# Optimization experiments

Measured on AMD Instinct MI355X. Metric: run time of the kernel, lower is better.

## Reference

```python
import jax, jax.numpy as jnp
import numpy as np

N_NODES = 100000
N_EDGES = 400000
DIMS = 384
LEAKY_SLOPE = 0.01  # torch LeakyReLU default


def _gcn_conv(x, src, dst, W, b, n_nodes):
    """PyG GCNConv: add self-loops, symmetric deg^{-1/2} normalization,
    linear transform, scatter-add aggregation to target nodes, bias."""
    loop = jnp.arange(n_nodes, dtype=src.dtype)
    src_a = jnp.concatenate([src, loop])
    dst_a = jnp.concatenate([dst, loop])
    deg = jax.ops.segment_sum(jnp.ones_like(dst_a, dtype=x.dtype), dst_a,
                              num_segments=n_nodes)
    dinv = jnp.where(deg > 0, jax.lax.rsqrt(deg), 0.0)
    norm = dinv[src_a] * dinv[dst_a]  # [E+N]
    h = x @ W  # [N, out]
    msg = norm[:, None] * h[src_a]  # gather + scale, [E+N, out]
    out = jax.ops.segment_sum(msg, dst_a, num_segments=n_nodes)  # scatter-add
    return out + b


def _leaky_relu(x):
    return jnp.where(x >= 0, x, LEAKY_SLOPE * x)


def setup_inputs() -> dict:
    key = jax.random.key(0)
    ks = jax.random.split(key, 8)
    d = DIMS
    x = jax.random.normal(ks[0], (N_NODES, d), dtype=jnp.float32)
    edge_index = jax.random.randint(ks[1], (2, N_EDGES), 0, N_NODES, dtype=jnp.int32)
    s1 = 1.0 / np.sqrt(d)
    s2 = 1.0 / np.sqrt(2 * d)
    W1 = jax.random.uniform(ks[2], (d, d), jnp.float32, -s1, s1)
    b1 = jnp.zeros((d,), jnp.float32)
    W2 = jax.random.uniform(ks[3], (2 * d, d), jnp.float32, -s2, s2)
    b2 = jnp.zeros((d,), jnp.float32)
    Wp = jax.random.uniform(ks[4], (d, 1), jnp.float32, -s1, s1)
    bp = jax.random.uniform(ks[5], (1,), jnp.float32, -s1, s1)
    return {"x": x, "edge_index": edge_index, "W1": W1, "b1": b1,
            "W2": W2, "b2": b2, "Wp": Wp, "bp": bp}


def reference(x, edge_index, W1, b1, W2, b2, Wp, bp):
    src, dst = edge_index[0], edge_index[1]
    n = x.shape[0]
    y = _gcn_conv(x, src, dst, W1, b1, n)            # [N, d]
    y = _leaky_relu(jnp.concatenate([x, y], axis=-1))  # [N, 2d]
    z = _leaky_relu(_gcn_conv(y, src, dst, W2, b2, n))  # [N, d]
    a = z @ Wp + bp                                   # [N, 1] pooler
    return (z, a)
```

## Files before the change

kernel.cpp:

```cpp
#include <hip/hip_runtime.h>

#define DIMS 384
#define SLOPE 0.01f

typedef __attribute__((ext_vector_type(8))) short s16x8;
typedef __attribute__((ext_vector_type(8))) unsigned short u16x8;
typedef __attribute__((ext_vector_type(4))) float f32x4;

typedef __attribute__((address_space(1))) const void gld_src_t;
typedef __attribute__((address_space(3))) void lds_dst_t;
#define GLL16(g, l) __builtin_amdgcn_global_load_lds((gld_src_t*)(g), (lds_dst_t*)(l), 16, 0, 0)

__device__ __forceinline__ unsigned short f2bf(float f) {
  unsigned u = __float_as_uint(f);
  unsigned r = (u + 0x7FFFu + ((u >> 16) & 1u)) >> 16;
  return (unsigned short)r;
}

__device__ __forceinline__ float bf2f(unsigned short u) {
  return __uint_as_float((unsigned)u << 16);
}

__device__ __forceinline__ float leaky(float f) { return f >= 0.f ? f : SLOPE * f; }


__global__ void count_kernel(const int* __restrict__ dst, int* __restrict__ cnt, int E) {
  int e = blockIdx.x * blockDim.x + threadIdx.x;
  if (e < E) atomicAdd(&cnt[dst[e]], 1);
}

__global__ void dinv_kernel(const int* __restrict__ cnt, float* __restrict__ dinv, int n) {
  int i = blockIdx.x * blockDim.x + threadIdx.x;
  if (i < n) dinv[i] = 1.0f / sqrtf((float)(cnt[i] + 1));
}

__global__ void scan1_kernel(const int* __restrict__ cnt, int* __restrict__ off,
                             int* __restrict__ bsum, int n) {
  __shared__ int s[256];
  int tid = threadIdx.x, gid = blockIdx.x * 256 + tid;
  int v = gid < n ? cnt[gid] : 0;
  s[tid] = v;
  __syncthreads();
  for (int o = 1; o < 256; o <<= 1) {
    int t = tid >= o ? s[tid - o] : 0;
    __syncthreads();
    s[tid] += t;
    __syncthreads();
  }
  if (gid < n) off[gid] = s[tid] - v;
  if (tid == 255) bsum[blockIdx.x] = s[255];
}

__global__ void scan2_kernel(const int* __restrict__ bsum, int* __restrict__ boff, int nb) {
  __shared__ int s[512];
  int tid = threadIdx.x;
  int v = tid < nb ? bsum[tid] : 0;
  s[tid] = v;
  __syncthreads();
  for (int o = 1; o < 512; o <<= 1) {
    int t = tid >= o ? s[tid - o] : 0;
    __syncthreads();
    s[tid] += t;
    __syncthreads();
  }
  if (tid < nb) boff[tid] = s[tid] - v;
}

__global__ void scan3_kernel(int* __restrict__ off, const int* __restrict__ boff,
                             int* __restrict__ cursor, int n, int E) {
  int gid = blockIdx.x * 256 + threadIdx.x;
  if (gid < n) {
    int v = off[gid] + boff[gid >> 8];
    off[gid] = v;
    cursor[gid] = v;
  }
  if (gid == 0) off[n] = E;
}

__global__ void fill_kernel(const int* __restrict__ src, const int* __restrict__ dst,
                            const float* __restrict__ dinv, int* __restrict__ cursor,
                            int* __restrict__ csr_s, float* __restrict__ csr_w, int E) {
  int e = blockIdx.x * blockDim.x + threadIdx.x;
  if (e >= E) return;
  int d = dst[e], s = src[e];
  int p = atomicAdd(&cursor[d], 1);
  csr_s[p] = s;
  csr_w[p] = dinv[s] * dinv[d];
}

__global__ void wt_kernel(const float* __restrict__ W, unsigned short* __restrict__ Wt, int K) {
  int idx = blockIdx.x * blockDim.x + threadIdx.x;
  if (idx >= K * DIMS) return;
  int k = idx / DIMS, nn = idx - k * DIMS;
  Wt[nn * K + k] = f2bf(W[idx]);
}

__global__ void xprep_kernel(const float* __restrict__ X, unsigned short* __restrict__ Xb,
                             unsigned short* __restrict__ XbL, int total8) {
  int i = blockIdx.x * blockDim.x + threadIdx.x;
  if (i >= total8) return;
  const float4* p = (const float4*)(X + (size_t)i * 8);
  float4 a = p[0], b = p[1];
  float f[8] = {a.x, a.y, a.z, a.w, b.x, b.y, b.z, b.w};
  u16x8 r, l;
#pragma unroll
  for (int j = 0; j < 8; j++) {
    r[j] = f2bf(f[j]);
    l[j] = f2bf(leaky(f[j]));
  }
  *(u16x8*)(Xb + (size_t)i * 8) = r;
  *(u16x8*)(XbL + (size_t)i * 8) = l;
}


template <int LAYER>
__launch_bounds__(256, 4)
__global__ void gemm_kernel(const unsigned short* __restrict__ A1,
                            const unsigned short* __restrict__ A2,
                            const unsigned short* __restrict__ Wt,
                            void* __restrict__ Hout, int M, int K) {
  __shared__ unsigned short As[128 * 64];
  __shared__ unsigned short Bs[128 * 64];
  const int tid = threadIdx.x;
  const int lane = tid & 63;
  const int wave = tid >> 6;
  const int wr = (wave >> 1) * 64;
  const int wc = (wave & 1) * 64;
  const int row0 = blockIdx.x * 128;
  const int n0 = blockIdx.y * 128;
  const int fr = lane & 15;
  const int kq = (lane >> 4) * 8;

  f32x4 acc[4][4] = {};

  for (int k0 = 0; k0 < K; k0 += 64) {
    __syncthreads();
    const unsigned short* Asrc;
    int ka;
    if (LAYER == 2 && k0 >= DIMS) {
      Asrc = A2;
      ka = k0 - DIMS;
    } else {
      Asrc = A1;
      ka = k0;
    }
#pragma unroll
    for (int i = 0; i < 4; i++) {
      const int g = i * 256 + tid;
      const int r = g >> 3;
      const int c = (g & 7) * 8;
      GLL16(Asrc + (size_t)(row0 + r) * DIMS + ka + c, &As[g * 8]);
    }
#pragma unroll
    for (int i = 0; i < 4; i++) {
      const int g = i * 256 + tid;
      const int r = g >> 3;
      const int c = (g & 7) * 8;
      GLL16(Wt + (size_t)(n0 + r) * K + k0 + c, &Bs[g * 8]);
    }
    __syncthreads();

#pragma unroll
    for (int h = 0; h < 2; h++) {
      s16x8 av[4], bv[4];
#pragma unroll
      for (int m = 0; m < 4; m++)
        av[m] = *(const s16x8*)&As[(wr + m * 16 + fr) * 64 + h * 32 + kq];
#pragma unroll
      for (int n = 0; n < 4; n++)
        bv[n] = *(const s16x8*)&Bs[(wc + n * 16 + fr) * 64 + h * 32 + kq];
#pragma unroll
      for (int m = 0; m < 4; m++)
#pragma unroll
        for (int n = 0; n < 4; n++)
          acc[m][n] = __builtin_amdgcn_mfma_f32_16x16x32_bf16(av[m], bv[n], acc[m][n], 0, 0, 0);
    }
  }

  const int rq = (lane >> 4) * 4;
#pragma unroll
  for (int m = 0; m < 4; m++) {
#pragma unroll
    for (int n = 0; n < 4; n++) {
      const int col = n0 + wc + n * 16 + fr;
#pragma unroll
      for (int j = 0; j < 4; j++) {
        const int row = row0 + wr + m * 16 + rq + j;
        if (row < M) {
          if (LAYER == 1)
            ((unsigned short*)Hout)[(size_t)row * DIMS + col] = f2bf(acc[m][n][j]);
          else
            ((float*)Hout)[(size_t)row * DIMS + col] = acc[m][n][j];
        }
      }
    }
  }
}


__global__ void agg1_kernel(const unsigned short* __restrict__ H, const float* __restrict__ bias,
                            const float* __restrict__ dinv, const int* __restrict__ off,
                            const int* __restrict__ csr_s, const float* __restrict__ csr_w,
                            unsigned short* __restrict__ Y, int n) {
  const int wid = (blockIdx.x * blockDim.x + threadIdx.x) >> 6;
  const int lane = threadIdx.x & 63;
  if (wid >= n) return;
  const float ds = dinv[wid];
  const float ws = ds * ds;
  const unsigned short* hr = H + (size_t)wid * DIMS;
  float acc[6];
#pragma unroll
  for (int j = 0; j < 3; j++) {
    const int d = 2 * lane + 128 * j;
    unsigned v = *(const unsigned*)(hr + d);
    acc[2 * j] = bias[d] + ws * bf2f((unsigned short)v);
    acc[2 * j + 1] = bias[d + 1] + ws * bf2f((unsigned short)(v >> 16));
  }
  const int e1 = off[wid + 1];
  for (int e = off[wid]; e < e1; e++) {
    const int s = csr_s[e];
    const float w = csr_w[e];
    const unsigned short* hs = H + (size_t)s * DIMS;
#pragma unroll
    for (int j = 0; j < 3; j++) {
      unsigned v = *(const unsigned*)(hs + 2 * lane + 128 * j);
      acc[2 * j] += w * bf2f((unsigned short)v);
      acc[2 * j + 1] += w * bf2f((unsigned short)(v >> 16));
    }
  }
  unsigned short* o = Y + (size_t)wid * DIMS;
#pragma unroll
  for (int j = 0; j < 3; j++) {
    unsigned lo = f2bf(leaky(acc[2 * j]));
    unsigned hi = f2bf(leaky(acc[2 * j + 1]));
    *(unsigned*)(o + 2 * lane + 128 * j) = lo | (hi << 16);
  }
}


__global__ void agg2_kernel(const float* __restrict__ H, const float* __restrict__ bias,
                            const float* __restrict__ dinv, const int* __restrict__ off,
                            const int* __restrict__ csr_s, const float* __restrict__ csr_w,
                            float* __restrict__ Z, const float* __restrict__ Wp,
                            const float* __restrict__ bp, float* __restrict__ A, int n) {
  const int wid = (blockIdx.x * blockDim.x + threadIdx.x) >> 6;
  const int lane = threadIdx.x & 63;
  if (wid >= n) return;
  const float ds = dinv[wid];
  const float ws = ds * ds;
  const float2* hr = (const float2*)(H + (size_t)wid * DIMS);
  float acc[6];
#pragma unroll
  for (int j = 0; j < 3; j++) {
    const int d = 2 * (lane + 64 * j);
    float2 v = hr[lane + 64 * j];
    acc[2 * j] = bias[d] + ws * v.x;
    acc[2 * j + 1] = bias[d + 1] + ws * v.y;
  }
  const int e1 = off[wid + 1];
  for (int e = off[wid]; e < e1; e++) {
    const int s = csr_s[e];
    const float w = csr_w[e];
    const float2* hs = (const float2*)(H + (size_t)s * DIMS);
#pragma unroll
    for (int j = 0; j < 3; j++) {
      float2 v = hs[lane + 64 * j];
      acc[2 * j] += w * v.x;
      acc[2 * j + 1] += w * v.y;
    }
  }
  float2* zr = (float2*)(Z + (size_t)wid * DIMS);
  float dot = 0.f;
#pragma unroll
  for (int j = 0; j < 3; j++) {
    float z0 = leaky(acc[2 * j]);
    float z1 = leaky(acc[2 * j + 1]);
    float2 wp = ((const float2*)Wp)[lane + 64 * j];
    zr[lane + 64 * j] = make_float2(z0, z1);
    dot += z0 * wp.x + z1 * wp.y;
  }
#pragma unroll
  for (int o = 32; o > 0; o >>= 1) dot += __shfl_xor(dot, o);
  if (lane == 0) A[wid] = dot + bp[0];
}


extern "C" void kernel_launch(void* const* d_in, const int* in_sizes, int n_in,
                              void* d_out, int out_size, void* d_ws, size_t ws_size,
                              hipStream_t stream) {
  const float* x = (const float*)d_in[0];
  const int* ei = (const int*)d_in[1];
  const float* W1 = (const float*)d_in[2];
  const float* b1 = (const float*)d_in[3];
  const float* W2 = (const float*)d_in[4];
  const float* b2 = (const float*)d_in[5];
  const float* Wp = (const float*)d_in[6];
  const float* bp = (const float*)d_in[7];
  const int N = in_sizes[0] / DIMS;
  const int E = in_sizes[1] / 2;
  const int* src = ei;
  const int* dst = ei + E;
  const int NP = N + 128;

  char* p = (char*)d_ws;
  auto alloc = [&](size_t bytes) {
    char* r = p;
    p += (bytes + 255) & ~(size_t)255;
    return r;
  };
  char* regionA = alloc(2 * (size_t)NP * DIMS * 2);
  unsigned short* Xb = (unsigned short*)regionA;
  unsigned short* H1 = (unsigned short*)(regionA + (size_t)NP * DIMS * 2);
  float* H2 = (float*)regionA;
  unsigned short* XbL = (unsigned short*)alloc((size_t)NP * DIMS * 2);
  unsigned short* YBL = (unsigned short*)alloc((size_t)NP * DIMS * 2);
  float* dinv = (float*)alloc((size_t)N * 4);
  int* cnt = (int*)alloc((size_t)N * 4);
  int* off = (int*)alloc((size_t)(N + 1) * 4);
  int* cursor = (int*)alloc((size_t)N * 4);
  int* bsum = (int*)alloc(4096);
  int* boff = (int*)alloc(4096);
  int* csr_s = (int*)alloc((size_t)E * 4);
  float* csr_w = (float*)alloc((size_t)E * 4);
  unsigned short* Wt1 = (unsigned short*)alloc((size_t)DIMS * DIMS * 2);
  unsigned short* Wt2 = (unsigned short*)alloc((size_t)DIMS * 2 * DIMS * 2);

  float* z = (float*)d_out;
  float* a = z + (size_t)N * DIMS;

  const int nbN = (N + 255) / 256;
  const int nbE = (E + 255) / 256;

  hipMemsetAsync(cnt, 0, (size_t)N * 4, stream);
  count_kernel<<<nbE, 256, 0, stream>>>(dst, cnt, E);
  dinv_kernel<<<nbN, 256, 0, stream>>>(cnt, dinv, N);
  scan1_kernel<<<nbN, 256, 0, stream>>>(cnt, off, bsum, N);
  scan2_kernel<<<1, 512, 0, stream>>>(bsum, boff, nbN);
  scan3_kernel<<<nbN, 256, 0, stream>>>(off, boff, cursor, N, E);
  fill_kernel<<<nbE, 256, 0, stream>>>(src, dst, dinv, cursor, csr_s, csr_w, E);
  wt_kernel<<<(DIMS * DIMS + 255) / 256, 256, 0, stream>>>(W1, Wt1, DIMS);
  wt_kernel<<<(2 * DIMS * DIMS + 255) / 256, 256, 0, stream>>>(W2, Wt2, 2 * DIMS);
  const int total8 = N * DIMS / 8;
  xprep_kernel<<<(total8 + 255) / 256, 256, 0, stream>>>(x, Xb, XbL, total8);

  dim3 gg((N + 127) / 128, DIMS / 128);
  gemm_kernel<1><<<gg, 256, 0, stream>>>(Xb, nullptr, Wt1, H1, N, DIMS);
  agg1_kernel<<<(N + 3) / 4, 256, 0, stream>>>(H1, b1, dinv, off, csr_s, csr_w, YBL, N);
  gemm_kernel<2><<<gg, 256, 0, stream>>>(XbL, YBL, Wt2, H2, N, 2 * DIMS);
  agg2_kernel<<<(N + 3) / 4, 256, 0, stream>>>(H2, b2, dinv, off, csr_s, csr_w, z, Wp, bp, a, N);
}
```

Baseline: 486.0 us.

## Store layer-2 features in bf16, replace scan with atomic offsets, unroll aggregation

The layer-2 GEMM output is now stored in bf16 instead of fp32, which halves the bytes gathered per edge in the second aggregation. The three-kernel prefix scan is replaced by a single kernel that reserves each node's CSR segment with an atomicAdd on a global counter, so segments are no longer in node order. Both aggregation kernels are merged into one template that processes two edges per iteration for more loads in flight, and the final z output uses nontemporal stores. The costs are lower precision in the layer-2 messages and scattered CSR locality from the atomic ordering.

```diff
diff --git a/kernel.cpp b/kernel.cpp
--- a/kernel.cpp
+++ b/kernel.cpp
@@ -6,6 +6,7 @@
 typedef __attribute__((ext_vector_type(8))) short s16x8;
 typedef __attribute__((ext_vector_type(8))) unsigned short u16x8;
 typedef __attribute__((ext_vector_type(4))) float f32x4;
+typedef __attribute__((ext_vector_type(2))) float f32x2;
 
 typedef __attribute__((address_space(1))) const void gld_src_t;
 typedef __attribute__((address_space(3))) void lds_dst_t;
@@ -29,52 +30,16 @@
   if (e < E) atomicAdd(&cnt[dst[e]], 1);
 }
 
-__global__ void dinv_kernel(const int* __restrict__ cnt, float* __restrict__ dinv, int n) {
+__global__ void node_prep_kernel(const int* __restrict__ cnt, int* __restrict__ tot,
+                                 float* __restrict__ dinv, int* __restrict__ off,
+                                 int* __restrict__ cursor, int n) {
   int i = blockIdx.x * blockDim.x + threadIdx.x;
-  if (i < n) dinv[i] = 1.0f / sqrtf((float)(cnt[i] + 1));
-}
-
-__global__ void scan1_kernel(const int* __restrict__ cnt, int* __restrict__ off,
-                             int* __restrict__ bsum, int n) {
-  __shared__ int s[256];
-  int tid = threadIdx.x, gid = blockIdx.x * 256 + tid;
-  int v = gid < n ? cnt[gid] : 0;
-  s[tid] = v;
-  __syncthreads();
-  for (int o = 1; o < 256; o <<= 1) {
-    int t = tid >= o ? s[tid - o] : 0;
-    __syncthreads();
-    s[tid] += t;
-    __syncthreads();
-  }
-  if (gid < n) off[gid] = s[tid] - v;
-  if (tid == 255) bsum[blockIdx.x] = s[255];
-}
-
-__global__ void scan2_kernel(const int* __restrict__ bsum, int* __restrict__ boff, int nb) {
-  __shared__ int s[512];
-  int tid = threadIdx.x;
-  int v = tid < nb ? bsum[tid] : 0;
-  s[tid] = v;
-  __syncthreads();
-  for (int o = 1; o < 512; o <<= 1) {
-    int t = tid >= o ? s[tid - o] : 0;
-    __syncthreads();
-    s[tid] += t;
-    __syncthreads();
-  }
-  if (tid < nb) boff[tid] = s[tid] - v;
-}
-
-__global__ void scan3_kernel(int* __restrict__ off, const int* __restrict__ boff,
-                             int* __restrict__ cursor, int n, int E) {
-  int gid = blockIdx.x * 256 + threadIdx.x;
-  if (gid < n) {
-    int v = off[gid] + boff[gid >> 8];
-    off[gid] = v;
-    cursor[gid] = v;
-  }
-  if (gid == 0) off[n] = E;
+  if (i >= n) return;
+  int c = cnt[i];
+  dinv[i] = 1.0f / sqrtf((float)(c + 1));
+  int o = atomicAdd(tot, c);
+  off[i] = o;
+  cursor[i] = o;
 }
 
 __global__ void fill_kernel(const int* __restrict__ src, const int* __restrict__ dst,
@@ -118,7 +83,7 @@
 __global__ void gemm_kernel(const unsigned short* __restrict__ A1,
                             const unsigned short* __restrict__ A2,
                             const unsigned short* __restrict__ Wt,
-                            void* __restrict__ Hout, int M, int K) {
+                            unsigned short* __restrict__ Hout, int M, int K) {
   __shared__ unsigned short As[128 * 64];
   __shared__ unsigned short Bs[128 * 64];
   const int tid = threadIdx.x;
@@ -186,22 +151,20 @@
 #pragma unroll
       for (int j = 0; j < 4; j++) {
         const int row = row0 + wr + m * 16 + rq + j;
-        if (row < M) {
-          if (LAYER == 1)
-            ((unsigned short*)Hout)[(size_t)row * DIMS + col] = f2bf(acc[m][n][j]);
-          else
-            ((float*)Hout)[(size_t)row * DIMS + col] = acc[m][n][j];
-        }
+        if (row < M) Hout[(size_t)row * DIMS + col] = f2bf(acc[m][n][j]);
       }
     }
   }
 }
 
 
-__global__ void agg1_kernel(const unsigned short* __restrict__ H, const float* __restrict__ bias,
-                            const float* __restrict__ dinv, const int* __restrict__ off,
-                            const int* __restrict__ csr_s, const float* __restrict__ csr_w,
-                            unsigned short* __restrict__ Y, int n) {
+template <int MODE>
+__global__ void agg_kernel(const unsigned short* __restrict__ H, const float* __restrict__ bias,
+                           const float* __restrict__ dinv, const int* __restrict__ off,
+                           const int* __restrict__ cnt, const int* __restrict__ csr_s,
+                           const float* __restrict__ csr_w, void* __restrict__ outp,
+                           const float* __restrict__ Wp, const float* __restrict__ bp,
+                           float* __restrict__ A, int n) {
   const int wid = (blockIdx.x * blockDim.x + threadIdx.x) >> 6;
   const int lane = threadIdx.x & 63;
   if (wid >= n) return;
@@ -216,8 +179,28 @@
     acc[2 * j] = bias[d] + ws * bf2f((unsigned short)v);
     acc[2 * j + 1] = bias[d + 1] + ws * bf2f((unsigned short)(v >> 16));
   }
-  const int e1 = off[wid + 1];
-  for (int e = off[wid]; e < e1; e++) {
+  const int e0 = off[wid];
+  const int e1 = e0 + cnt[wid];
+  int e = e0;
+  for (; e + 2 <= e1; e += 2) {
+    const int sA = csr_s[e], sB = csr_s[e + 1];
+    const float wA = csr_w[e], wB = csr_w[e + 1];
+    const unsigned short* hA = H + (size_t)sA * DIMS;
+    const unsigned short* hB = H + (size_t)sB * DIMS;
+    unsigned vA[3], vB[3];
+#pragma unroll
+    for (int j = 0; j < 3; j++) vA[j] = *(const unsigned*)(hA + 2 * lane + 128 * j);
+#pragma unroll
+    for (int j = 0; j < 3; j++) vB[j] = *(const unsigned*)(hB + 2 * lane + 128 * j);
+#pragma unroll
+    for (int j = 0; j < 3; j++) {
+      acc[2 * j] += wA * bf2f((unsigned short)vA[j]);
+      acc[2 * j + 1] += wA * bf2f((unsigned short)(vA[j] >> 16));
+      acc[2 * j] += wB * bf2f((unsigned short)vB[j]);
+      acc[2 * j + 1] += wB * bf2f((unsigned short)(vB[j] >> 16));
+    }
+  }
+  if (e < e1) {
     const int s = csr_s[e];
     const float w = csr_w[e];
     const unsigned short* hs = H + (size_t)s * DIMS;
@@ -228,60 +211,30 @@
       acc[2 * j + 1] += w * bf2f((unsigned short)(v >> 16));
     }
   }
-  unsigned short* o = Y + (size_t)wid * DIMS;
-#pragma unroll
-  for (int j = 0; j < 3; j++) {
-    unsigned lo = f2bf(leaky(acc[2 * j]));
-    unsigned hi = f2bf(leaky(acc[2 * j + 1]));
-    *(unsigned*)(o + 2 * lane + 128 * j) = lo | (hi << 16);
-  }
-}
-
-
-__global__ void agg2_kernel(const float* __restrict__ H, const float* __restrict__ bias,
-                            const float* __restrict__ dinv, const int* __restrict__ off,
-                            const int* __restrict__ csr_s, const float* __restrict__ csr_w,
-                            float* __restrict__ Z, const float* __restrict__ Wp,
-                            const float* __restrict__ bp, float* __restrict__ A, int n) {
-  const int wid = (blockIdx.x * blockDim.x + threadIdx.x) >> 6;
-  const int lane = threadIdx.x & 63;
-  if (wid >= n) return;
-  const float ds = dinv[wid];
-  const float ws = ds * ds;
-  const float2* hr = (const float2*)(H + (size_t)wid * DIMS);
-  float acc[6];
-#pragma unroll
-  for (int j = 0; j < 3; j++) {
-    const int d = 2 * (lane + 64 * j);
-    float2 v = hr[lane + 64 * j];
-    acc[2 * j] = bias[d] + ws * v.x;
-    acc[2 * j + 1] = bias[d + 1] + ws * v.y;
-  }
-  const int e1 = off[wid + 1];
-  for (int e = off[wid]; e < e1; e++) {
-    const int s = csr_s[e];
-    const float w = csr_w[e];
-    const float2* hs = (const float2*)(H + (size_t)s * DIMS);
+  if (MODE == 1) {
+    unsigned short* o = (unsigned short*)outp + (size_t)wid * DIMS;
 #pragma unroll
     for (int j = 0; j < 3; j++) {
-      float2 v = hs[lane + 64 * j];
-      acc[2 * j] += w * v.x;
-      acc[2 * j + 1] += w * v.y;
-    }
-  }
-  float2* zr = (float2*)(Z + (size_t)wid * DIMS);
-  float dot = 0.f;
-#pragma unroll
-  for (int j = 0; j < 3; j++) {
-    float z0 = leaky(acc[2 * j]);
-    float z1 = leaky(acc[2 * j + 1]);
-    float2 wp = ((const float2*)Wp)[lane + 64 * j];
-    zr[lane + 64 * j] = make_float2(z0, z1);
-    dot += z0 * wp.x + z1 * wp.y;
-  }
-#pragma unroll
-  for (int o = 32; o > 0; o >>= 1) dot += __shfl_xor(dot, o);
-  if (lane == 0) A[wid] = dot + bp[0];
+      unsigned lo = f2bf(leaky(acc[2 * j]));
+      unsigned hi = f2bf(leaky(acc[2 * j + 1]));
+      *(unsigned*)(o + 2 * lane + 128 * j) = lo | (hi << 16);
+    }
+  } else {
+    float* Z = (float*)outp + (size_t)wid * DIMS;
+    float dot = 0.f;
+#pragma unroll
+    for (int j = 0; j < 3; j++) {
+      float z0 = leaky(acc[2 * j]);
+      float z1 = leaky(acc[2 * j + 1]);
+      f32x2 wp = *(const f32x2*)(Wp + 2 * lane + 128 * j);
+      f32x2 zv = {z0, z1};
+      __builtin_nontemporal_store(zv, (f32x2*)(Z + 2 * lane + 128 * j));
+      dot += z0 * wp.x + z1 * wp.y;
+    }
+#pragma unroll
+    for (int o = 32; o > 0; o >>= 1) dot += __shfl_xor(dot, o);
+    if (lane == 0) A[wid] = dot + bp[0];
+  }
 }
 
 
@@ -311,15 +264,14 @@
   char* regionA = alloc(2 * (size_t)NP * DIMS * 2);
   unsigned short* Xb = (unsigned short*)regionA;
   unsigned short* H1 = (unsigned short*)(regionA + (size_t)NP * DIMS * 2);
-  float* H2 = (float*)regionA;
+  unsigned short* H2 = (unsigned short*)regionA;
   unsigned short* XbL = (unsigned short*)alloc((size_t)NP * DIMS * 2);
   unsigned short* YBL = (unsigned short*)alloc((size_t)NP * DIMS * 2);
   float* dinv = (float*)alloc((size_t)N * 4);
-  int* cnt = (int*)alloc((size_t)N * 4);
-  int* off = (int*)alloc((size_t)(N + 1) * 4);
+  int* cnt = (int*)alloc((size_t)(N + 1) * 4);
+  int* tot = cnt + N;
+  int* off = (int*)alloc((size_t)N * 4);
   int* cursor = (int*)alloc((size_t)N * 4);
-  int* bsum = (int*)alloc(4096);
-  int* boff = (int*)alloc(4096);
   int* csr_s = (int*)alloc((size_t)E * 4);
   float* csr_w = (float*)alloc((size_t)E * 4);
   unsigned short* Wt1 = (unsigned short*)alloc((size_t)DIMS * DIMS * 2);
@@ -331,12 +283,9 @@
   const int nbN = (N + 255) / 256;
   const int nbE = (E + 255) / 256;
 
-  hipMemsetAsync(cnt, 0, (size_t)N * 4, stream);
+  hipMemsetAsync(cnt, 0, (size_t)(N + 1) * 4, stream);
   count_kernel<<<nbE, 256, 0, stream>>>(dst, cnt, E);
-  dinv_kernel<<<nbN, 256, 0, stream>>>(cnt, dinv, N);
-  scan1_kernel<<<nbN, 256, 0, stream>>>(cnt, off, bsum, N);
-  scan2_kernel<<<1, 512, 0, stream>>>(bsum, boff, nbN);
-  scan3_kernel<<<nbN, 256, 0, stream>>>(off, boff, cursor, N, E);
+  node_prep_kernel<<<nbN, 256, 0, stream>>>(cnt, tot, dinv, off, cursor, N);
   fill_kernel<<<nbE, 256, 0, stream>>>(src, dst, dinv, cursor, csr_s, csr_w, E);
   wt_kernel<<<(DIMS * DIMS + 255) / 256, 256, 0, stream>>>(W1, Wt1, DIMS);
   wt_kernel<<<(2 * DIMS * DIMS + 255) / 256, 256, 0, stream>>>(W2, Wt2, 2 * DIMS);
@@ -345,7 +294,9 @@
 
   dim3 gg((N + 127) / 128, DIMS / 128);
   gemm_kernel<1><<<gg, 256, 0, stream>>>(Xb, nullptr, Wt1, H1, N, DIMS);
-  agg1_kernel<<<(N + 3) / 4, 256, 0, stream>>>(H1, b1, dinv, off, csr_s, csr_w, YBL, N);
+  agg_kernel<1><<<(N + 3) / 4, 256, 0, stream>>>(H1, b1, dinv, off, cnt, csr_s, csr_w, YBL,
+                                                 nullptr, nullptr, nullptr, N);
   gemm_kernel<2><<<gg, 256, 0, stream>>>(XbL, YBL, Wt2, H2, N, 2 * DIMS);
-  agg2_kernel<<<(N + 3) / 4, 256, 0, stream>>>(H2, b2, dinv, off, csr_s, csr_w, z, Wp, bp, a, N);
-}
+  agg_kernel<2><<<(N + 3) / 4, 256, 0, stream>>>(H2, b2, dinv, off, cnt, csr_s, csr_w, z,
+                                                 Wp, bp, a, N);
+}
```

Measured after the change: 421.4 us. -13.3%, faster.
